# Optimization experiments

Hardware: AMD Instinct MI355X
Metric: run time of the kernel (lower is better)

Reference implementation:

```python
import jax, jax.numpy as jnp
import numpy as np

B, LQ, LK, H = 8, 2048, 2048, 1024


def setup_inputs() -> dict:
    key = jax.random.key(0)
    kq, kk, kv, km, kw = jax.random.split(key, 5)
    input_Q = jax.random.normal(kq, (B, LQ, H), dtype=jnp.float32)
    input_K = jax.random.normal(kk, (B, LK, H), dtype=jnp.float32)
    input_V = jax.random.normal(kv, (B, LK, H), dtype=jnp.float32)
    mask = jax.random.randint(km, (B, LK), 0, 2, dtype=jnp.int32)
    # learned parameter w_omega [H, H]; scaled init so scores are O(1)-ish
    w_omega = jax.random.normal(kw, (H, H), dtype=jnp.float32) * (H ** -0.5)
    return {"input_Q": input_Q, "input_K": input_K, "input_V": input_V,
            "w_omega": w_omega, "mask": mask}


def reference(input_Q, input_K, input_V, w_omega, mask):
    # att_input = Q @ W : [B, Lq, H]
    att_input = jnp.einsum('bqh,hd->bqd', input_Q, w_omega)
    # scores = att_input @ K^T : [B, Lq, Lk]
    att_scores = jnp.einsum('bqd,bkd->bqk', att_input, input_K)
    # masked fill with -inf where mask == 0 (mask broadcast over query dim)
    neg_inf = jnp.asarray(-jnp.inf, dtype=att_scores.dtype)
    scores = jnp.where(mask[:, None, :] == 0, neg_inf, att_scores)
    probs_softmax = jax.nn.softmax(scores, axis=-1)          # [B, Lq, Lk]
    probs_sigmoid = jax.nn.sigmoid(scores)                   # sigmoid(-inf)=0
    probs_sigmoid_hat = (probs_sigmoid > 0.5).astype(probs_softmax.dtype)
    att_output_softmax = jnp.einsum('bqk,bkh->bqh', probs_softmax, input_V)
    att_output_sigmoid = jnp.einsum('bqk,bkh->bqh', probs_sigmoid_hat, input_V)
    # torch .squeeze(1) is a no-op here since Lq > 1
    return (att_output_softmax, att_output_sigmoid, probs_softmax, probs_sigmoid)
```

## Files before the change

### kernel.cpp

```cpp
#include <hip/hip_runtime.h>
#include <math.h>

#define B_  8
#define LQ_ 2048
#define LK_ 2048
#define H_  1024

#define TAU      4e-3f
#define FIX_CAP  32768
#define FIX_E    8
#define SCL      256.0f
#define SCLQ     16.0f
#define INV_SS   (1.0f / 1048576.0f)

#define KBLK 512

typedef unsigned short ushort_t;
typedef __attribute__((ext_vector_type(8))) _Float16 v8h;
typedef __attribute__((ext_vector_type(4))) float  v4f;
typedef __attribute__((ext_vector_type(4))) float  f4;
typedef __attribute__((ext_vector_type(4))) int    i4;
typedef __attribute__((ext_vector_type(4))) short  s4;

#if defined(__has_builtin)
#if __has_builtin(__builtin_amdgcn_global_load_lds)
#define HAS_GLDS 1
#endif
#endif

__device__ __forceinline__ ushort_t f2bf(float x) {
  unsigned u = __float_as_uint(x);
  u = (u + 0x7FFFu + ((u >> 16) & 1u)) >> 16;
  return (ushort_t)u;
}
__device__ __forceinline__ void split2h(float x, ushort_t& h, ushort_t& l) {
  union { _Float16 f; ushort_t u; } a, b;
  a.f = (_Float16)x;
  b.f = (_Float16)(x - (float)a.f);
  h = a.u; l = b.u;
}

__device__ __forceinline__ void gld_lds16(void* lds_dst, const void* g_src) {
#ifdef HAS_GLDS
  __builtin_amdgcn_global_load_lds((const __attribute__((address_space(1))) void*)g_src,
                                   (__attribute__((address_space(3))) void*)lds_dst,
                                   16, 0, 0);
#else
  *(i4*)lds_dst = *(const i4*)g_src;
#endif
}

__global__ void k_zero(int* p) { *p = 0; }

__global__ void k_split(const float* __restrict__ x, ushort_t* __restrict__ hi,
                        ushort_t* __restrict__ lo, int n4, float scale) {
  int stride = gridDim.x * blockDim.x;
  for (int i = blockIdx.x * blockDim.x + threadIdx.x; i < n4; i += stride) {
    f4 v = ((const f4*)x)[i];
    s4 h, l;
#pragma unroll
    for (int j = 0; j < 4; j++) {
      ushort_t hb, lb; split2h(v[j] * scale, hb, lb);
      h[j] = (short)hb; l[j] = (short)lb;
    }
    ((s4*)hi)[i] = h;
    ((s4*)lo)[i] = l;
  }
}

template <int SPLIT>
__global__ void k_transpose(const float* __restrict__ X, ushort_t* __restrict__ Yhi,
                            ushort_t* __restrict__ Ylo, int R, int C, float scale) {
  __shared__ float t[32][33];
  const int b = blockIdx.z;
  const float* Xb = X + (size_t)b * R * C;
  ushort_t* Yh = Yhi + (size_t)b * R * C;
  const int c0 = blockIdx.x * 32, r0 = blockIdx.y * 32;
  const int tx = threadIdx.x, ty = threadIdx.y;
#pragma unroll
  for (int i = 0; i < 4; i++)
    t[ty + 8 * i][tx] = Xb[(size_t)(r0 + ty + 8 * i) * C + c0 + tx];
  __syncthreads();
#pragma unroll
  for (int i = 0; i < 4; i++) {
    float v = t[tx][ty + 8 * i] * scale;
    size_t o = (size_t)(c0 + ty + 8 * i) * R + r0 + tx;
    if (SPLIT) {
      ushort_t h, l; split2h(v, h, l);
      Yh[o] = h;
      (Ylo + (size_t)b * R * C)[o] = l;
    } else {
      Yh[o] = f2bf(v);
    }
  }
}

template <int EPI>
__global__ __launch_bounds__(256, 2)
void gemm_hx2(const ushort_t* __restrict__ Ahi, const ushort_t* __restrict__ Alo,
              const ushort_t* __restrict__ Bhi, const ushort_t* __restrict__ Blo,
              int KD, long strideAB, long strideBB, int N,
              ushort_t* __restrict__ OutHi, ushort_t* __restrict__ OutLo, long strideOB,
              float* __restrict__ S, float* __restrict__ G, const int* __restrict__ mask,
              int* __restrict__ cnt, int* __restrict__ flist) {
  const int b  = blockIdx.z;
  const int m0 = blockIdx.y * 128;
  const int n0 = blockIdx.x * 128;
  const ushort_t* Ah = Ahi + (size_t)b * strideAB + (size_t)m0 * KD;
  const ushort_t* Al = Alo + (size_t)b * strideAB + (size_t)m0 * KD;
  const ushort_t* Bh = Bhi + (size_t)b * strideBB + (size_t)n0 * KD;
  const ushort_t* Bl = Blo + (size_t)b * strideBB + (size_t)n0 * KD;

  __shared__ ushort_t sAh[128 * 32], sAl[128 * 32], sBh[128 * 32], sBl[128 * 32];

  const int tid  = threadIdx.x;
  const int lane = tid & 63;
  const int wid  = tid >> 6;
  const int wm   = (wid >> 1) * 64;
  const int wn   = (wid & 1) * 64;

  v4f acc[4][4] = {};

  const size_t go1 = (size_t)(tid >> 2) * KD + (size_t)((tid & 3) * 8);
  const size_t go2 = (size_t)((tid >> 2) + 64) * KD + (size_t)((tid & 3) * 8);
  const int ldst1 = tid * 16;
  const int ldst2 = 4096 + tid * 16;

  for (int k0 = 0; k0 < KD; k0 += 32) {
    __syncthreads();
    gld_lds16((char*)sAh + ldst1, Ah + go1 + k0);
    gld_lds16((char*)sAh + ldst2, Ah + go2 + k0);
    gld_lds16((char*)sAl + ldst1, Al + go1 + k0);
    gld_lds16((char*)sAl + ldst2, Al + go2 + k0);
    gld_lds16((char*)sBh + ldst1, Bh + go1 + k0);
    gld_lds16((char*)sBh + ldst2, Bh + go2 + k0);
    gld_lds16((char*)sBl + ldst1, Bl + go1 + k0);
    gld_lds16((char*)sBl + ldst2, Bl + go2 + k0);
    __syncthreads();

    const int fr = lane & 15;
    const int fk = (lane >> 4) * 8;
    v8h a_h[4], a_l[4], b_h[4], b_l[4];
#pragma unroll
    for (int i = 0; i < 4; i++) {
      a_h[i] = *(const v8h*)&sAh[(wm + i * 16 + fr) * 32 + fk];
      a_l[i] = *(const v8h*)&sAl[(wm + i * 16 + fr) * 32 + fk];
      b_h[i] = *(const v8h*)&sBh[(wn + i * 16 + fr) * 32 + fk];
      b_l[i] = *(const v8h*)&sBl[(wn + i * 16 + fr) * 32 + fk];
    }
#pragma unroll
    for (int i = 0; i < 4; i++)
#pragma unroll
      for (int j = 0; j < 4; j++) {
        acc[i][j] = __builtin_amdgcn_mfma_f32_16x16x32_f16(a_h[i], b_h[j], acc[i][j], 0, 0, 0);
        acc[i][j] = __builtin_amdgcn_mfma_f32_16x16x32_f16(a_h[i], b_l[j], acc[i][j], 0, 0, 0);
        acc[i][j] = __builtin_amdgcn_mfma_f32_16x16x32_f16(a_l[i], b_h[j], acc[i][j], 0, 0, 0);
      }
  }

  const int fr = lane & 15;
  const int rg = (lane >> 4) * 4;
#pragma unroll
  for (int i = 0; i < 4; i++)
#pragma unroll
    for (int j = 0; j < 4; j++)
#pragma unroll
      for (int r = 0; r < 4; r++) {
        const int grow = m0 + wm + i * 16 + rg + r;
        const int gcol = n0 + wn + j * 16 + fr;
        const float v = acc[i][j][r];
        if (EPI == 0) {
          size_t o = (size_t)b * strideOB + (size_t)grow * N + gcol;
          ushort_t h, l; split2h(v, h, l);
          OutHi[o] = h; OutLo[o] = l;
        } else {
          size_t o = ((size_t)b * LQ_ + grow) * N + gcol;
          const float sv = v * INV_SS;
          S[o] = sv;
          int mk = mask[b * N + gcol];
          G[o] = mk ? 1.0f / (1.0f + expf(-sv)) : 0.0f;
          if (mk && fabsf(sv) < TAU) {
            int idx = atomicAdd(cnt, 1);
            if (idx < FIX_CAP) flist[idx] = (b << 22) | (grow << 11) | gcol;
          }
        }
      }
}

__global__ __launch_bounds__(256)
void k_fix_blas(const int* __restrict__ cnt, const int* __restrict__ flist,
                const float* __restrict__ Q, const float* __restrict__ Kx,
                const float* __restrict__ W, float* __restrict__ S,
                float* __restrict__ G) {
  const int n = min(*cnt, FIX_CAP);
  const int base = blockIdx.x * FIX_E;
  if (base >= n) return;
  const int ne = min(FIX_E, n - base);
  const int tid = threadIdx.x;

  __shared__ float qs[FIX_E][H_];
  __shared__ float aA[FIX_E][H_];
  __shared__ int   ent[FIX_E];

  if (tid < FIX_E) ent[tid] = flist[base + ((tid < ne) ? tid : 0)];
  __syncthreads();

  for (int e = 0; e < FIX_E; e++) {
    const int en = ent[e];
    const int b = en >> 22, q = (en >> 11) & 2047;
    const float* Qr = Q + ((size_t)b * LQ_ + q) * H_;
    for (int i = tid; i < H_; i += 256) qs[e][i] = Qr[i];
  }
  __syncthreads();

  float atot[FIX_E][4];
  float acc[FIX_E][4];
  const float* Wp = W + tid * 4;
#pragma unroll
  for (int blk = 0; blk < 2; blk++) {
    const int h0 = blk * KBLK;
    const int h1 = h0 + KBLK;
#pragma unroll
    for (int e = 0; e < FIX_E; e++)
#pragma unroll
      for (int j = 0; j < 4; j++) acc[e][j] = 0.f;
    for (int h = h0; h < h1; h++) {
      f4 w = *(const f4*)(Wp + (size_t)h * H_);
#pragma unroll
      for (int e = 0; e < FIX_E; e++) {
        const float qv = qs[e][h];
        acc[e][0] = fmaf(qv, w[0], acc[e][0]);
        acc[e][1] = fmaf(qv, w[1], acc[e][1]);
        acc[e][2] = fmaf(qv, w[2], acc[e][2]);
        acc[e][3] = fmaf(qv, w[3], acc[e][3]);
      }
    }
#pragma unroll
    for (int e = 0; e < FIX_E; e++)
#pragma unroll
      for (int j = 0; j < 4; j++)
        atot[e][j] = (blk == 0) ? acc[e][j] : __fadd_rn(atot[e][j], acc[e][j]);
  }
#pragma unroll
  for (int e = 0; e < FIX_E; e++) {
    aA[e][tid * 4 + 0] = atot[e][0];
    aA[e][tid * 4 + 1] = atot[e][1];
    aA[e][tid * 4 + 2] = atot[e][2];
    aA[e][tid * 4 + 3] = atot[e][3];
  }
  __syncthreads();

  if (tid < ne) {
    const int e = tid;
    const int en = ent[e];
    const int b = en >> 22, q = (en >> 11) & 2047, k = en & 2047;
    const float* Kr = Kx + ((size_t)b * LK_ + k) * H_;
    const float* Ar = aA[e];
    float stot = 0.f;
#pragma unroll
    for (int blk = 0; blk < 2; blk++) {
      const int d0 = blk * KBLK;
      const int d1 = d0 + KBLK;
      float a = 0.f;
#pragma unroll 16
      for (int d = d0; d < d1; d++) a = fmaf(Ar[d], Kr[d], a);
      stot = (blk == 0) ? a : __fadd_rn(stot, a);
    }
    size_t o = ((size_t)b * LQ_ + q) * LK_ + k;
    S[o] = stot;
    G[o] = 1.0f / (1.0f + expf(-stot));
  }
}

__global__ void k_softmax(float* __restrict__ S, const int* __restrict__ mask) {
  const int row = blockIdx.x;
  const int b   = row >> 11;
  float* Sr = S + (size_t)row * LK_;
  const int* mr = mask + b * LK_;
  const int tid = threadIdx.x;
  const int c0 = tid * 8;

  float v[8]; int mk[8];
  f4 v0 = *(const f4*)&Sr[c0];
  f4 v1 = *(const f4*)&Sr[c0 + 4];
  i4 m0 = *(const i4*)&mr[c0];
  i4 m1 = *(const i4*)&mr[c0 + 4];
#pragma unroll
  for (int j = 0; j < 4; j++) { v[j] = v0[j]; v[4 + j] = v1[j]; mk[j] = m0[j]; mk[4 + j] = m1[j]; }

  float mx = -INFINITY;
#pragma unroll
  for (int j = 0; j < 8; j++) if (mk[j]) mx = fmaxf(mx, v[j]);
#pragma unroll
  for (int off = 32; off; off >>= 1) mx = fmaxf(mx, __shfl_xor(mx, off));
  __shared__ float redm[4], reds[4];
  const int lane = tid & 63, wid = tid >> 6;
  if (lane == 0) redm[wid] = mx;
  __syncthreads();
  mx = fmaxf(fmaxf(redm[0], redm[1]), fmaxf(redm[2], redm[3]));

  float e[8], sum = 0.f;
#pragma unroll
  for (int j = 0; j < 8; j++) { e[j] = mk[j] ? expf(v[j] - mx) : 0.f; sum += e[j]; }
#pragma unroll
  for (int off = 32; off; off >>= 1) sum += __shfl_xor(sum, off);
  if (lane == 0) reds[wid] = sum;
  __syncthreads();
  sum = reds[0] + reds[1] + reds[2] + reds[3];
  const float inv = 1.0f / sum;

  f4 o0, o1;
#pragma unroll
  for (int j = 0; j < 4; j++) { o0[j] = e[j] * inv; o1[j] = e[4 + j] * inv; }
  *(f4*)&Sr[c0] = o0;
  *(f4*)&Sr[c0 + 4] = o1;
}

typedef __attribute__((ext_vector_type(8))) short v8s;
template <int MODE>
__global__ __launch_bounds__(256, 2)
void gemm_pv(const float* __restrict__ A, const ushort_t* __restrict__ Bt,
             float* __restrict__ O) {
  const int b  = blockIdx.z;
  const int m0 = blockIdx.y * 128;
  const int n0 = blockIdx.x * 128;
  const float*    Ab = A  + ((size_t)b * LQ_ + m0) * LK_;
  const ushort_t* Bb = Bt + ((size_t)b * H_  + n0) * LK_;

  __shared__ ushort_t sA[128 * 32], sB[128 * 32];

  const int tid  = threadIdx.x;
  const int lane = tid & 63;
  const int wid  = tid >> 6;
  const int wm   = (wid >> 1) * 64;
  const int wn   = (wid & 1) * 64;

  v4f acc[4][4] = {};

  const int arow = tid >> 3;
  const int akq  = (tid & 7) * 4;
  const size_t bgo1 = (size_t)(tid >> 2) * LK_ + (size_t)((tid & 3) * 8);
  const size_t bgo2 = (size_t)((tid >> 2) + 64) * LK_ + (size_t)((tid & 3) * 8);

  for (int k0 = 0; k0 < LK_; k0 += 32) {
    __syncthreads();
    gld_lds16((char*)sB + tid * 16,        Bb + bgo1 + k0);
    gld_lds16((char*)sB + 4096 + tid * 16, Bb + bgo2 + k0);
#pragma unroll
    for (int it = 0; it < 4; it++) {
      const int r = arow + it * 32;
      f4 v = *(const f4*)&Ab[(size_t)r * LK_ + k0 + akq];
      s4 sv;
#pragma unroll
      for (int j = 0; j < 4; j++) {
        if (MODE)
          sv[j] = (short)((v[j] > 0.5f) ? 0x3F80 : 0);
        else
          sv[j] = (short)f2bf(v[j]);
      }
      *(s4*)&sA[r * 32 + akq] = sv;
    }
    __syncthreads();

    const int fr = lane & 15;
    const int fk = (lane >> 4) * 8;
    v8s af[4], bf[4];
#pragma unroll
    for (int i = 0; i < 4; i++) {
      af[i] = *(const v8s*)&sA[(wm + i * 16 + fr) * 32 + fk];
      bf[i] = *(const v8s*)&sB[(wn + i * 16 + fr) * 32 + fk];
    }
#pragma unroll
    for (int i = 0; i < 4; i++)
#pragma unroll
      for (int j = 0; j < 4; j++)
        acc[i][j] = __builtin_amdgcn_mfma_f32_16x16x32_bf16(af[i], bf[j], acc[i][j], 0, 0, 0);
  }

  const int fr = lane & 15;
  const int rg = (lane >> 4) * 4;
#pragma unroll
  for (int i = 0; i < 4; i++)
#pragma unroll
    for (int j = 0; j < 4; j++)
#pragma unroll
      for (int r = 0; r < 4; r++) {
        const int grow = m0 + wm + i * 16 + rg + r;
        const int gcol = n0 + wn + j * 16 + fr;
        O[((size_t)b * LQ_ + grow) * H_ + gcol] = acc[i][j][r];
      }
}

extern "C" void kernel_launch(void* const* d_in, const int* in_sizes, int n_in,
                              void* d_out, int out_size, void* d_ws, size_t ws_size,
                              hipStream_t stream) {
  const float* Q = (const float*)d_in[0];
  const float* K = (const float*)d_in[1];
  const float* V = (const float*)d_in[2];
  const float* W = (const float*)d_in[3];
  const int* mask = (const int*)d_in[4];

  float* out0 = (float*)d_out;
  float* out1 = out0 + (size_t)B_ * LQ_ * H_;
  float* out2 = out1 + (size_t)B_ * LQ_ * H_;
  float* out3 = out2 + (size_t)B_ * LQ_ * LK_;

  const size_t NQ = (size_t)B_ * LQ_ * H_;
  char* ws = (char*)d_ws;
  int* cnt   = (int*)ws;                    ws += 256;
  int* flist = (int*)ws;                    ws += FIX_CAP * 4;
  ushort_t* Qhi = (ushort_t*)ws;            ws += NQ * 2;
  ushort_t* Qlo = (ushort_t*)ws;            ws += NQ * 2;
  ushort_t* Khi = (ushort_t*)ws;            ws += NQ * 2;
  ushort_t* Klo = (ushort_t*)ws;            ws += NQ * 2;
  ushort_t* Ahi = (ushort_t*)ws;            ws += NQ * 2;
  ushort_t* Alo = (ushort_t*)ws;            ws += NQ * 2;
  ushort_t* Vt  = (ushort_t*)ws;            ws += NQ * 2;
  ushort_t* Wthi = (ushort_t*)ws;           ws += (size_t)H_ * H_ * 2;
  ushort_t* Wtlo = (ushort_t*)ws;

  k_zero<<<1, 1, 0, stream>>>(cnt);

  k_split<<<2048, 256, 0, stream>>>(Q, Qhi, Qlo, (int)(NQ / 4), SCLQ);
  k_split<<<2048, 256, 0, stream>>>(K, Khi, Klo, (int)(NQ / 4), SCL);
  dim3 tb(32, 8);
  k_transpose<1><<<dim3(32, 32, 1), tb, 0, stream>>>(W, Wthi, Wtlo, H_, H_, SCL);
  k_transpose<0><<<dim3(32, 64, B_), tb, 0, stream>>>(V, Vt, nullptr, LK_, H_, 1.0f);

  gemm_hx2<0><<<dim3(H_ / 128, LQ_ / 128, B_), 256, 0, stream>>>(
      Qhi, Qlo, Wthi, Wtlo, H_, (long)LQ_ * H_, 0L, H_,
      Ahi, Alo, (long)LQ_ * H_, nullptr, nullptr, nullptr, nullptr, nullptr);

  gemm_hx2<1><<<dim3(LK_ / 128, LQ_ / 128, B_), 256, 0, stream>>>(
      Ahi, Alo, Khi, Klo, H_, (long)LQ_ * H_, (long)LK_ * H_, LK_,
      nullptr, nullptr, 0L, out2, out3, mask, cnt, flist);

  k_fix_blas<<<FIX_CAP / FIX_E, 256, 0, stream>>>(cnt, flist, Q, K, W, out2, out3);

  gemm_pv<1><<<dim3(H_ / 128, LQ_ / 128, B_), 256, 0, stream>>>(out3, Vt, out1);

  k_softmax<<<B_ * LQ_, 256, 0, stream>>>(out2, mask);

  gemm_pv<0><<<dim3(H_ / 128, LQ_ / 128, B_), 256, 0, stream>>>(out2, Vt, out0);
}
```

Measured before the change: 1.032 ms.

## Emit bf16 probability copies upstream and XOR-swizzle LDS tiles in GEMMs

The score GEMM epilogue and fix kernel now also write a bf16 thresholded sigmoid-hat matrix, and the softmax kernel writes a bf16 copy of the probabilities. The PV GEMMs can then load A directly with global-to-LDS loads instead of reading fp32 and converting in registers. This halves A-operand read traffic in the PV GEMMs at the cost of extra bf16 writes in the producers. Both GEMM kernels also get an XOR swizzle on LDS column chunks to reduce bank conflicts, and the bf16 copies reuse dead workspace buffers (Qhi, Ahi).

New measurement: 963.6 us. -6.7%, faster.

```diff
diff --git a/kernel.cpp b/kernel.cpp
--- a/kernel.cpp
+++ b/kernel.cpp
@@ -17,6 +17,7 @@
 
 typedef unsigned short ushort_t;
 typedef __attribute__((ext_vector_type(8))) _Float16 v8h;
+typedef __attribute__((ext_vector_type(8))) short  v8s;
 typedef __attribute__((ext_vector_type(4))) float  v4f;
 typedef __attribute__((ext_vector_type(4))) float  f4;
 typedef __attribute__((ext_vector_type(4))) int    i4;
@@ -95,14 +96,15 @@
   }
 }
 
+
 template <int EPI>
 __global__ __launch_bounds__(256, 2)
 void gemm_hx2(const ushort_t* __restrict__ Ahi, const ushort_t* __restrict__ Alo,
               const ushort_t* __restrict__ Bhi, const ushort_t* __restrict__ Blo,
               int KD, long strideAB, long strideBB, int N,
               ushort_t* __restrict__ OutHi, ushort_t* __restrict__ OutLo, long strideOB,
-              float* __restrict__ S, float* __restrict__ G, const int* __restrict__ mask,
-              int* __restrict__ cnt, int* __restrict__ flist) {
+              float* __restrict__ S, float* __restrict__ G, ushort_t* __restrict__ Hatb,
+              const int* __restrict__ mask, int* __restrict__ cnt, int* __restrict__ flist) {
   const int b  = blockIdx.z;
   const int m0 = blockIdx.y * 128;
   const int n0 = blockIdx.x * 128;
@@ -121,10 +123,15 @@
 
   v4f acc[4][4] = {};
 
-  const size_t go1 = (size_t)(tid >> 2) * KD + (size_t)((tid & 3) * 8);
-  const size_t go2 = (size_t)((tid >> 2) + 64) * KD + (size_t)((tid & 3) * 8);
+  const int r1 = tid >> 2;
+  const int c1 = (tid & 3) ^ ((tid >> 3) & 3);
+  const size_t go1 = (size_t)r1 * KD + (size_t)(c1 * 8);
+  const size_t go2 = (size_t)(r1 + 64) * KD + (size_t)(c1 * 8);
   const int ldst1 = tid * 16;
   const int ldst2 = 4096 + tid * 16;
+
+  const int fr = lane & 15;
+  const int cq = lane >> 4;
 
   for (int k0 = 0; k0 < KD; k0 += 32) {
     __syncthreads();
@@ -138,15 +145,17 @@
     gld_lds16((char*)sBl + ldst2, Bl + go2 + k0);
     __syncthreads();
 
-    const int fr = lane & 15;
-    const int fk = (lane >> 4) * 8;
     v8h a_h[4], a_l[4], b_h[4], b_l[4];
 #pragma unroll
     for (int i = 0; i < 4; i++) {
-      a_h[i] = *(const v8h*)&sAh[(wm + i * 16 + fr) * 32 + fk];
-      a_l[i] = *(const v8h*)&sAl[(wm + i * 16 + fr) * 32 + fk];
-      b_h[i] = *(const v8h*)&sBh[(wn + i * 16 + fr) * 32 + fk];
-      b_l[i] = *(const v8h*)&sBl[(wn + i * 16 + fr) * 32 + fk];
+      const int Ra = wm + i * 16 + fr;
+      const int ca = Ra * 32 + (((cq ^ ((Ra >> 1) & 3))) << 3);
+      a_h[i] = *(const v8h*)&sAh[ca];
+      a_l[i] = *(const v8h*)&sAl[ca];
+      const int Rb = wn + i * 16 + fr;
+      const int cb = Rb * 32 + (((cq ^ ((Rb >> 1) & 3))) << 3);
+      b_h[i] = *(const v8h*)&sBh[cb];
+      b_l[i] = *(const v8h*)&sBl[cb];
     }
 #pragma unroll
     for (int i = 0; i < 4; i++)
@@ -158,7 +167,6 @@
       }
   }
 
-  const int fr = lane & 15;
   const int rg = (lane >> 4) * 4;
 #pragma unroll
   for (int i = 0; i < 4; i++)
@@ -178,7 +186,9 @@
           const float sv = v * INV_SS;
           S[o] = sv;
           int mk = mask[b * N + gcol];
-          G[o] = mk ? 1.0f / (1.0f + expf(-sv)) : 0.0f;
+          const float g = mk ? 1.0f / (1.0f + expf(-sv)) : 0.0f;
+          G[o] = g;
+          Hatb[o] = (g > 0.5f) ? (ushort_t)0x3F80 : (ushort_t)0;
           if (mk && fabsf(sv) < TAU) {
             int idx = atomicAdd(cnt, 1);
             if (idx < FIX_CAP) flist[idx] = (b << 22) | (grow << 11) | gcol;
@@ -191,7 +201,7 @@
 void k_fix_blas(const int* __restrict__ cnt, const int* __restrict__ flist,
                 const float* __restrict__ Q, const float* __restrict__ Kx,
                 const float* __restrict__ W, float* __restrict__ S,
-                float* __restrict__ G) {
+                float* __restrict__ G, ushort_t* __restrict__ Hatb) {
   const int n = min(*cnt, FIX_CAP);
   const int base = blockIdx.x * FIX_E;
   if (base >= n) return;
@@ -268,11 +278,14 @@
     }
     size_t o = ((size_t)b * LQ_ + q) * LK_ + k;
     S[o] = stot;
-    G[o] = 1.0f / (1.0f + expf(-stot));
-  }
-}
-
-__global__ void k_softmax(float* __restrict__ S, const int* __restrict__ mask) {
+    const float g = 1.0f / (1.0f + expf(-stot));
+    G[o] = g;
+    Hatb[o] = (g > 0.5f) ? (ushort_t)0x3F80 : (ushort_t)0;
+  }
+}
+
+__global__ void k_softmax(float* __restrict__ S, const int* __restrict__ mask,
+                          ushort_t* __restrict__ Pb) {
   const int row = blockIdx.x;
   const int b   = row >> 11;
   float* Sr = S + (size_t)row * LK_;
@@ -310,22 +323,25 @@
   const float inv = 1.0f / sum;
 
   f4 o0, o1;
-#pragma unroll
-  for (int j = 0; j < 4; j++) { o0[j] = e[j] * inv; o1[j] = e[4 + j] * inv; }
+  v8s pb;
+#pragma unroll
+  for (int j = 0; j < 4; j++) {
+    o0[j] = e[j] * inv; o1[j] = e[4 + j] * inv;
+    pb[j] = (short)f2bf(o0[j]); pb[4 + j] = (short)f2bf(o1[j]);
+  }
   *(f4*)&Sr[c0] = o0;
   *(f4*)&Sr[c0 + 4] = o1;
-}
-
-typedef __attribute__((ext_vector_type(8))) short v8s;
-template <int MODE>
+  *(v8s*)&Pb[(size_t)row * LK_ + c0] = pb;
+}
+
 __global__ __launch_bounds__(256, 2)
-void gemm_pv(const float* __restrict__ A, const ushort_t* __restrict__ Bt,
-             float* __restrict__ O) {
+void gemm_pvb(const ushort_t* __restrict__ A, const ushort_t* __restrict__ Bt,
+              float* __restrict__ O) {
   const int b  = blockIdx.z;
   const int m0 = blockIdx.y * 128;
   const int n0 = blockIdx.x * 128;
-  const float*    Ab = A  + ((size_t)b * LQ_ + m0) * LK_;
-  const ushort_t* Bb = Bt + ((size_t)b * H_  + n0) * LK_;
+  const ushort_t* Ab = A  + ((size_t)b * LQ_ + m0) * (size_t)LK_;
+  const ushort_t* Bb = Bt + ((size_t)b * H_  + n0) * (size_t)LK_;
 
   __shared__ ushort_t sA[128 * 32], sB[128 * 32];
 
@@ -337,38 +353,31 @@
 
   v4f acc[4][4] = {};
 
-  const int arow = tid >> 3;
-  const int akq  = (tid & 7) * 4;
-  const size_t bgo1 = (size_t)(tid >> 2) * LK_ + (size_t)((tid & 3) * 8);
-  const size_t bgo2 = (size_t)((tid >> 2) + 64) * LK_ + (size_t)((tid & 3) * 8);
+  const int r1 = tid >> 2;
+  const int c1 = (tid & 3) ^ ((tid >> 3) & 3);
+  const size_t go1 = (size_t)r1 * LK_ + (size_t)(c1 * 8);
+  const size_t go2 = (size_t)(r1 + 64) * LK_ + (size_t)(c1 * 8);
+  const int ldst1 = tid * 16;
+  const int ldst2 = 4096 + tid * 16;
+
+  const int fr = lane & 15;
+  const int cq = lane >> 4;
 
   for (int k0 = 0; k0 < LK_; k0 += 32) {
     __syncthreads();
-    gld_lds16((char*)sB + tid * 16,        Bb + bgo1 + k0);
-    gld_lds16((char*)sB + 4096 + tid * 16, Bb + bgo2 + k0);
-#pragma unroll
-    for (int it = 0; it < 4; it++) {
-      const int r = arow + it * 32;
-      f4 v = *(const f4*)&Ab[(size_t)r * LK_ + k0 + akq];
-      s4 sv;
-#pragma unroll
-      for (int j = 0; j < 4; j++) {
-        if (MODE)
-          sv[j] = (short)((v[j] > 0.5f) ? 0x3F80 : 0);
-        else
-          sv[j] = (short)f2bf(v[j]);
-      }
-      *(s4*)&sA[r * 32 + akq] = sv;
-    }
+    gld_lds16((char*)sA + ldst1, Ab + go1 + k0);
+    gld_lds16((char*)sA + ldst2, Ab + go2 + k0);
+    gld_lds16((char*)sB + ldst1, Bb + go1 + k0);
+    gld_lds16((char*)sB + ldst2, Bb + go2 + k0);
     __syncthreads();
 
-    const int fr = lane & 15;
-    const int fk = (lane >> 4) * 8;
     v8s af[4], bf[4];
 #pragma unroll
     for (int i = 0; i < 4; i++) {
-      af[i] = *(const v8s*)&sA[(wm + i * 16 + fr) * 32 + fk];
-      bf[i] = *(const v8s*)&sB[(wn + i * 16 + fr) * 32 + fk];
+      const int Ra = wm + i * 16 + fr;
+      af[i] = *(const v8s*)&sA[Ra * 32 + ((cq ^ ((Ra >> 1) & 3)) << 3)];
+      const int Rb = wn + i * 16 + fr;
+      bf[i] = *(const v8s*)&sB[Rb * 32 + ((cq ^ ((Rb >> 1) & 3)) << 3)];
     }
 #pragma unroll
     for (int i = 0; i < 4; i++)
@@ -377,7 +386,6 @@
         acc[i][j] = __builtin_amdgcn_mfma_f32_16x16x32_bf16(af[i], bf[j], acc[i][j], 0, 0, 0);
   }
 
-  const int fr = lane & 15;
   const int rg = (lane >> 4) * 4;
 #pragma unroll
   for (int i = 0; i < 4; i++)
@@ -419,6 +427,9 @@
   ushort_t* Wthi = (ushort_t*)ws;           ws += (size_t)H_ * H_ * 2;
   ushort_t* Wtlo = (ushort_t*)ws;
 
+  ushort_t* hatb = Qhi;
+  ushort_t* Pb   = Ahi;
+
   k_zero<<<1, 1, 0, stream>>>(cnt);
 
   k_split<<<2048, 256, 0, stream>>>(Q, Qhi, Qlo, (int)(NQ / 4), SCLQ);
@@ -429,17 +440,17 @@
 
   gemm_hx2<0><<<dim3(H_ / 128, LQ_ / 128, B_), 256, 0, stream>>>(
       Qhi, Qlo, Wthi, Wtlo, H_, (long)LQ_ * H_, 0L, H_,
-      Ahi, Alo, (long)LQ_ * H_, nullptr, nullptr, nullptr, nullptr, nullptr);
+      Ahi, Alo, (long)LQ_ * H_, nullptr, nullptr, nullptr, nullptr, nullptr, nullptr);
 
   gemm_hx2<1><<<dim3(LK_ / 128, LQ_ / 128, B_), 256, 0, stream>>>(
       Ahi, Alo, Khi, Klo, H_, (long)LQ_ * H_, (long)LK_ * H_, LK_,
-      nullptr, nullptr, 0L, out2, out3, mask, cnt, flist);
-
-  k_fix_blas<<<FIX_CAP / FIX_E, 256, 0, stream>>>(cnt, flist, Q, K, W, out2, out3);
-
-  gemm_pv<1><<<dim3(H_ / 128, LQ_ / 128, B_), 256, 0, stream>>>(out3, Vt, out1);
-
-  k_softmax<<<B_ * LQ_, 256, 0, stream>>>(out2, mask);
-
-  gemm_pv<0><<<dim3(H_ / 128, LQ_ / 128, B_), 256, 0, stream>>>(out2, Vt, out0);
-}
+      nullptr, nullptr, 0L, out2, out3, hatb, mask, cnt, flist);
+
+  k_fix_blas<<<FIX_CAP / FIX_E, 256, 0, stream>>>(cnt, flist, Q, K, W, out2, out3, hatb);
+
+  gemm_pvb<<<dim3(H_ / 128, LQ_ / 128, B_), 256, 0, stream>>>(hatb, Vt, out1);
+
+  k_softmax<<<B_ * LQ_, 256, 0, stream>>>(out2, mask, Pb);
+
+  gemm_pvb<<<dim3(H_ / 128, LQ_ / 128, B_), 256, 0, stream>>>(Pb, Vt, out0);
+}
```
